# Kernel optimization log

Hardware: AMD Instinct MI355X
Metric: run time of the kernel (lower is better)

Reference implementation:

```python
import jax, jax.numpy as jnp
import numpy as np

V, P, C, M, P_ORIG, T = 81920, 131072, 512, 1024, 163840, 262144


def setup_inputs() -> dict:
    key = jax.random.key(0)
    ks = jax.random.split(key, 6)
    adapter_feat = jax.random.normal(ks[0], (V, C), dtype=jnp.float32)
    ce = jax.random.normal(ks[1], (M, C), dtype=jnp.float32)
    # caption embeddings arrive pre-normalized in the original pipeline
    caption_embed = ce / jnp.clip(jnp.linalg.norm(ce, axis=-1, keepdims=True), 1e-12)
    logit_scale = jnp.full((1,), np.log(1.0 / 0.07), dtype=jnp.float32)  # learnable param init
    v2p_map = jax.random.randint(ks[2], (P,), 0, V, dtype=jnp.int32)
    origin_idx = jax.random.randint(ks[3], (P,), 0, P_ORIG, dtype=jnp.int32)
    caption_to_point_mapping = jax.random.randint(ks[4], (T,), 0, P_ORIG, dtype=jnp.int32)
    caption_seg_idx = jnp.sort(jax.random.randint(ks[5], (T,), 0, M, dtype=jnp.int32))
    return {
        "adapter_feat": adapter_feat,
        "caption_embed": caption_embed,
        "logit_scale": logit_scale,
        "v2p_map": v2p_map,
        "origin_idx": origin_idx,
        "caption_to_point_mapping": caption_to_point_mapping,
        "caption_seg_idx": caption_seg_idx,
        "n_origin_points": P_ORIG,
    }


def reference(adapter_feat, caption_embed, logit_scale, v2p_map, origin_idx,
              caption_to_point_mapping, caption_seg_idx, n_origin_points):
    n_pts = v2p_map.shape[0]
    n_captions = caption_embed.shape[0]

    # gather voxel features to points, L2-normalize (feat_norm=True)
    feats = adapter_feat[v2p_map]                                       # [P, C]
    feats = feats / jnp.clip(jnp.linalg.norm(feats, axis=-1, keepdims=True), 1e-12)

    # per-point log-softmax caption scores
    logits = (feats @ caption_embed.T) * jnp.exp(logit_scale[0])        # [P, M]
    scores = jax.nn.log_softmax(logits, axis=-1)                        # [P, M]

    # origin-point -> current-point mapping; -1 where origin point was dropped
    ptom = jnp.full((n_origin_points,), -1, dtype=jnp.int32)
    ptom = ptom.at[origin_idx].set(jnp.arange(n_pts, dtype=jnp.int32))

    gidx = ptom[caption_to_point_mapping]                               # [T]
    invalid = (gidx < 0).astype(scores.dtype)                           # [T]
    # torch negative advanced indexing wraps; replicate faithfully
    safe = jnp.where(gidx < 0, gidx + n_pts, gidx)
    gathered = scores[safe]                                             # [T, M]

    # scatter-sum scores and counts per caption segment
    pooled = jax.ops.segment_sum(gathered, caption_seg_idx, num_segments=n_captions)
    cnt = jax.ops.segment_sum(jnp.ones_like(invalid), caption_seg_idx, num_segments=n_captions)
    ninv = jax.ops.segment_sum(invalid, caption_seg_idx, num_segments=n_captions)
    real_n_points = cnt - ninv                                          # [N]

    denom = jnp.where(real_n_points > 0,
                      1.0 / jnp.where(real_n_points > 0, real_n_points, 1.0), 0.0)
    pooled = pooled * denom[:, None]                                    # [N, M]
    if_has_pts = real_n_points > 0
    return pooled, real_n_points, if_has_pts
```

## Files before the change

kernel.cpp:

```cpp
#include <hip/hip_runtime.h>

#define P_PTS 131072
#define CDIM  512
#define MCAP  1024
#define TLEN  262144
#define PORIG 163840

typedef unsigned short u16;
typedef unsigned char  u8;
typedef __attribute__((ext_vector_type(8))) short short8;
typedef __attribute__((ext_vector_type(4))) float f32x4;
typedef __attribute__((ext_vector_type(8))) int int8v;
typedef __attribute__((ext_vector_type(4))) int int4v;

__device__ __forceinline__ u16 f2bf(float f) {
    unsigned u = __float_as_uint(f);
    unsigned r = (u + 0x7FFFu + ((u >> 16) & 1u)) >> 16;
    return (u16)r;
}
__device__ __forceinline__ float d_e4m3(unsigned x) {
    float f = __uint_as_float((x & 0x7Fu) << 20) * 0x1p120f;
    return __uint_as_float(__float_as_uint(f) | ((x & 0x80u) << 24));
}
__device__ __forceinline__ void ld16(const void* g, void* l) {
    __builtin_amdgcn_global_load_lds(
        (const __attribute__((address_space(1))) void*)g,
        (__attribute__((address_space(3))) void*)l, 16, 0, 0);
}

__global__ __launch_bounds__(256) void prep(const float* __restrict__ cap,
                                            const int* __restrict__ oidx,
                                            u16* __restrict__ capb,
                                            u8* __restrict__ cap8,
                                            int* __restrict__ ptom,
                                            float* __restrict__ lse_sum) {
    int b = blockIdx.x, tid = threadIdx.x;
    if (b < 512) {
        int i = (b * 256 + tid) * 4;
        float4 v = *(const float4*)(cap + i);
        u16* o = capb + i;
        o[0] = f2bf(v.x); o[1] = f2bf(v.y); o[2] = f2bf(v.z); o[3] = f2bf(v.w);
        int p = __builtin_amdgcn_cvt_pk_fp8_f32(v.x, v.y, 0, false);
        p = __builtin_amdgcn_cvt_pk_fp8_f32(v.z, v.w, p, true);
        *(int*)(cap8 + i) = p;
        int t = b * 256 + tid;
        atomicMax(&ptom[oidx[t]], t);
    } else {
        int j = (b - 512) * 256 + tid;
        lse_sum[j] = 0.0f;
    }
}

__global__ __launch_bounds__(256) void gather_normalize(
    const float* __restrict__ adapter, const int* __restrict__ v2p,
    u8* __restrict__ feats8) {
    int p = blockIdx.x * 4 + (threadIdx.x >> 6);
    int lane = threadIdx.x & 63;
    int vrow = v2p[p];
    const float4* src = (const float4*)(adapter + (size_t)vrow * CDIM);
    float4 x0 = src[lane * 2];
    float4 x1 = src[lane * 2 + 1];
    float ss = x0.x*x0.x + x0.y*x0.y + x0.z*x0.z + x0.w*x0.w
             + x1.x*x1.x + x1.y*x1.y + x1.z*x1.z + x1.w*x1.w;
    #pragma unroll
    for (int off = 32; off >= 1; off >>= 1) ss += __shfl_xor(ss, off, 64);
    float inv = 1.0f / fmaxf(sqrtf(ss), 1e-12f);
    int lo = __builtin_amdgcn_cvt_pk_fp8_f32(x0.x*inv, x0.y*inv, 0, false);
    lo = __builtin_amdgcn_cvt_pk_fp8_f32(x0.z*inv, x0.w*inv, lo, true);
    int hi = __builtin_amdgcn_cvt_pk_fp8_f32(x1.x*inv, x1.y*inv, 0, false);
    hi = __builtin_amdgcn_cvt_pk_fp8_f32(x1.z*inv, x1.w*inv, hi, true);
    uint2 w; w.x = (unsigned)lo; w.y = (unsigned)hi;
    *(uint2*)(feats8 + (size_t)p * CDIM + lane * 8) = w;
}

__global__ __launch_bounds__(256) void make_rows(const int* __restrict__ ctpm,
                                                 const int* __restrict__ ptom,
                                                 unsigned* __restrict__ rows) {
    int t = blockIdx.x * 256 + threadIdx.x;
    int g = ptom[ctpm[t]];
    rows[t] = (g < 0) ? ((unsigned)(g + P_PTS) | 0x80000000u) : (unsigned)g;
}

__global__ __launch_bounds__(256) void lse_gemm(
    const u8* __restrict__ feats8, const u8* __restrict__ cap8,
    const float* __restrict__ lsc, float* __restrict__ lse_sum) {
    __shared__ __align__(16) u8 As[16384];
    __shared__ __align__(16) u8 Bs[16384];
    const int tid  = threadIdx.x;
    const int wave = tid >> 6;
    const int lane = tid & 63;
    const unsigned id = blockIdx.x;
    const int col0 = (int)((id >> 3) & 7u) * 128;
    const int row0 = (int)((id & 7u) + 8u * (id >> 6)) * 128;
    const int wm = (wave >> 1) * 64;
    const int wn = (wave & 1) * 64;
    const float sf = __expf(lsc[0]);

    f32x4 acc[4][4] = {};

    const int srow = tid >> 3;
    const int kc   = (tid & 7) ^ (srow & 7);
    const u8* gA = feats8 + (size_t)(row0 + srow) * CDIM + kc * 16;
    const u8* gB = cap8   + (size_t)(col0 + srow) * CDIM + kc * 16;
    u8* lA = As + wave * 1024;
    u8* lB = Bs + wave * 1024;

    const int m = lane & 15;
    const int q = lane >> 4;
    const u8* rA1 = As + (size_t)((wm + m) * 8 + ((2*q)   ^ (m & 7))) * 16;
    const u8* rA2 = As + (size_t)((wm + m) * 8 + ((2*q+1) ^ (m & 7))) * 16;
    const u8* rB1 = Bs + (size_t)((wn + m) * 8 + ((2*q)   ^ (m & 7))) * 16;
    const u8* rB2 = Bs + (size_t)((wn + m) * 8 + ((2*q+1) ^ (m & 7))) * 16;

    #pragma unroll
    for (int k0 = 0; k0 < CDIM; k0 += 128) {
        __syncthreads();
        #pragma unroll
        for (int c = 0; c < 4; ++c) {
            ld16(gA + (size_t)c * 32 * CDIM + k0, lA + c * 4096);
            ld16(gB + (size_t)c * 32 * CDIM + k0, lB + c * 4096);
        }
        __syncthreads();
        int8v af[4], bv[4];
        #pragma unroll
        for (int i = 0; i < 4; ++i) {
            int4v lo = *(const int4v*)(rA1 + i * 2048);
            int4v hi = *(const int4v*)(rA2 + i * 2048);
            af[i][0]=lo[0]; af[i][1]=lo[1]; af[i][2]=lo[2]; af[i][3]=lo[3];
            af[i][4]=hi[0]; af[i][5]=hi[1]; af[i][6]=hi[2]; af[i][7]=hi[3];
        }
        #pragma unroll
        for (int j = 0; j < 4; ++j) {
            int4v lo = *(const int4v*)(rB1 + j * 2048);
            int4v hi = *(const int4v*)(rB2 + j * 2048);
            bv[j][0]=lo[0]; bv[j][1]=lo[1]; bv[j][2]=lo[2]; bv[j][3]=lo[3];
            bv[j][4]=hi[0]; bv[j][5]=hi[1]; bv[j][6]=hi[2]; bv[j][7]=hi[3];
        }
        #pragma unroll
        for (int i = 0; i < 4; ++i)
            #pragma unroll
            for (int j = 0; j < 4; ++j)
                acc[i][j] = __builtin_amdgcn_mfma_scale_f32_16x16x128_f8f6f4(
                    af[i], bv[j], acc[i][j], 0, 0, 0, 127, 0, 127);
    }

    #pragma unroll
    for (int i = 0; i < 4; ++i) {
        float s4[4] = {0.f, 0.f, 0.f, 0.f};
        #pragma unroll
        for (int j = 0; j < 4; ++j)
            #pragma unroll
            for (int r = 0; r < 4; ++r)
                s4[r] += __expf(acc[i][j][r] * sf - sf);
        #pragma unroll
        for (int off = 8; off >= 1; off >>= 1)
            #pragma unroll
            for (int r = 0; r < 4; ++r)
                s4[r] += __shfl_xor(s4[r], off, 64);
        if (m == 0) {
            int rbase = row0 + wm + i * 16 + q * 4;
            #pragma unroll
            for (int r = 0; r < 4; ++r)
                atomicAdd(&lse_sum[rbase + r], s4[r]);
        }
    }
}

__device__ __forceinline__ int lower_bound(const int* __restrict__ a, int n, int key) {
    int lo = 0, hi = n;
    while (lo < hi) { int mid = (lo + hi) >> 1; if (a[mid] < key) lo = mid + 1; else hi = mid; }
    return lo;
}

__global__ __launch_bounds__(1024) void seg_reduce(
    const u8* __restrict__ feats8, const float* __restrict__ lse_sum,
    const unsigned* __restrict__ rows, const int* __restrict__ seg,
    const float* __restrict__ lsc,
    u16* __restrict__ Fb, float* __restrict__ Lout, float* __restrict__ realn) {
    int s = blockIdx.x;
    int tid = threadIdx.x, wave = tid >> 6, lane = tid & 63;
    int start = lower_bound(seg, TLEN, s);
    int end   = lower_bound(seg, TLEN, s + 1);
    float a[8] = {0,0,0,0,0,0,0,0};
    float Lacc = 0.f; int inv = 0;
    int r = start + wave;
    for (; r + 16 < end; r += 32) {
        unsigned p0 = rows[r], p1 = rows[r + 16];
        int r0 = (int)(p0 & 0x7FFFFFFFu), r1 = (int)(p1 & 0x7FFFFFFFu);
        uint2 v0 = *(const uint2*)(feats8 + (size_t)r0 * CDIM + lane * 8);
        uint2 v1 = *(const uint2*)(feats8 + (size_t)r1 * CDIM + lane * 8);
        if (lane == 0) {
            inv += (int)(p0 >> 31) + (int)(p1 >> 31);
            Lacc += __logf(lse_sum[r0]) + __logf(lse_sum[r1]);
        }
        a[0] += d_e4m3(v0.x);       a[1] += d_e4m3(v0.x >> 8);
        a[2] += d_e4m3(v0.x >> 16); a[3] += d_e4m3(v0.x >> 24);
        a[4] += d_e4m3(v0.y);       a[5] += d_e4m3(v0.y >> 8);
        a[6] += d_e4m3(v0.y >> 16); a[7] += d_e4m3(v0.y >> 24);
        a[0] += d_e4m3(v1.x);       a[1] += d_e4m3(v1.x >> 8);
        a[2] += d_e4m3(v1.x >> 16); a[3] += d_e4m3(v1.x >> 24);
        a[4] += d_e4m3(v1.y);       a[5] += d_e4m3(v1.y >> 8);
        a[6] += d_e4m3(v1.y >> 16); a[7] += d_e4m3(v1.y >> 24);
    }
    if (r < end) {
        unsigned p0 = rows[r];
        int r0 = (int)(p0 & 0x7FFFFFFFu);
        uint2 v0 = *(const uint2*)(feats8 + (size_t)r0 * CDIM + lane * 8);
        if (lane == 0) { inv += (int)(p0 >> 31); Lacc += __logf(lse_sum[r0]); }
        a[0] += d_e4m3(v0.x);       a[1] += d_e4m3(v0.x >> 8);
        a[2] += d_e4m3(v0.x >> 16); a[3] += d_e4m3(v0.x >> 24);
        a[4] += d_e4m3(v0.y);       a[5] += d_e4m3(v0.y >> 8);
        a[6] += d_e4m3(v0.y >> 16); a[7] += d_e4m3(v0.y >> 24);
    }
    __shared__ float pF[16][512];
    __shared__ float pL[16];
    __shared__ int   pI[16];
    #pragma unroll
    for (int u = 0; u < 8; ++u) pF[wave][lane * 8 + u] = a[u];
    if (lane == 0) { pL[wave] = Lacc; pI[wave] = inv; }
    __syncthreads();
    if (tid < 512) {
        float f = 0.f;
        #pragma unroll
        for (int w = 0; w < 16; ++w) f += pF[w][tid];
        Fb[(size_t)s * CDIM + tid] = f2bf(f);
    }
    if (tid == 0) {
        float cnt = (float)(end - start);
        float Ls = 0.f; int ninv = 0;
        #pragma unroll
        for (int w = 0; w < 16; ++w) { Ls += pL[w]; ninv += pI[w]; }
        realn[s] = cnt - (float)ninv;
        Lout[s] = Ls + __expf(lsc[0]) * cnt;
    }
}

__global__ __launch_bounds__(256) void pooled_gemm(
    const u16* __restrict__ Fb, const u16* __restrict__ capb,
    const float* __restrict__ Lout, const float* __restrict__ realn,
    const float* __restrict__ lsc, float* __restrict__ out) {
    __shared__ __align__(16) u16 As[64 * 32];
    __shared__ __align__(16) u16 Bs[64 * 32];
    const int tid  = threadIdx.x;
    const int wave = tid >> 6;
    const int lane = tid & 63;
    const int col0 = blockIdx.x * 64;
    const int row0 = blockIdx.y * 64;
    const int wm = (wave >> 1) * 32;
    const int wn = (wave & 1) * 32;
    const float sf = __expf(lsc[0]);
    f32x4 acc[2][2] = {};
    const int srow = tid >> 2;
    const int scol = (tid & 3) * 8;
    const u16* gA0 = Fb   + (size_t)(row0 + srow) * CDIM + scol;
    const u16* gB0 = capb + (size_t)(col0 + srow) * CDIM + scol;
    u16* lA0 = As + wave * 512;
    u16* lB0 = Bs + wave * 512;
    const int mrow = lane & 15;
    const int quad = lane >> 4;
    const u16* rA = As + (wm + mrow) * 32 + quad * 8;
    const u16* rB = Bs + (wn + mrow) * 32 + quad * 8;
    #pragma unroll 4
    for (int k0 = 0; k0 < CDIM; k0 += 32) {
        __syncthreads();
        ld16(gA0 + k0, lA0);
        ld16(gB0 + k0, lB0);
        __syncthreads();
        short8 af[2], bfr[2];
        #pragma unroll
        for (int i = 0; i < 2; ++i) af[i]  = *(const short8*)(rA + i * 512);
        #pragma unroll
        for (int j = 0; j < 2; ++j) bfr[j] = *(const short8*)(rB + j * 512);
        #pragma unroll
        for (int i = 0; i < 2; ++i)
            #pragma unroll
            for (int j = 0; j < 2; ++j)
                acc[i][j] = __builtin_amdgcn_mfma_f32_16x16x32_bf16(
                    af[i], bfr[j], acc[i][j], 0, 0, 0);
    }
    #pragma unroll
    for (int i = 0; i < 2; ++i) {
        #pragma unroll
        for (int r = 0; r < 4; ++r) {
            int s = row0 + wm + i * 16 + quad * 4 + r;
            float rn = realn[s];
            float dn = rn > 0.f ? 1.0f / rn : 0.0f;
            float L = Lout[s];
            #pragma unroll
            for (int j = 0; j < 2; ++j) {
                int mc = col0 + wn + j * 16 + mrow;
                out[(size_t)s * MCAP + mc] = (sf * acc[i][j][r] - L) * dn;
            }
        }
    }
    if (col0 == 0 && tid < 64) {
        int s = row0 + tid;
        float rv = realn[s];
        out[MCAP * MCAP + s] = rv;
        out[MCAP * MCAP + MCAP + s] = (rv > 0.f) ? 1.0f : 0.0f;
    }
}

extern "C" void kernel_launch(void* const* d_in, const int* in_sizes, int n_in,
                              void* d_out, int out_size, void* d_ws, size_t ws_size,
                              hipStream_t stream) {
    const float* adapter = (const float*)d_in[0];
    const float* cap     = (const float*)d_in[1];
    const float* lsc     = (const float*)d_in[2];
    const int*   v2p     = (const int*)d_in[3];
    const int*   oidx    = (const int*)d_in[4];
    const int*   ctpm    = (const int*)d_in[5];
    const int*   seg     = (const int*)d_in[6];
    float* out = (float*)d_out;

    char* ws = (char*)d_ws;
    u8*       feats8  = (u8*)(ws);
    u8*       cap8    = (u8*)(ws + 67108864);
    u16*      capb    = (u16*)(ws + 67633152);
    float*    lse_sum = (float*)(ws + 68681728);
    int*      ptom    = (int*)(ws + 69206016);
    unsigned* rows    = (unsigned*)(ws + 69861376);
    u16*      Fb      = (u16*)(ws + 70909952);
    float*    Lout    = (float*)(ws + 71958528);
    float*    realn   = (float*)(ws + 71962624);

    hipMemsetAsync(ptom, 0xFF, (size_t)PORIG * 4, stream);

    prep<<<1024, 256, 0, stream>>>(cap, oidx, capb, cap8, ptom, lse_sum);
    gather_normalize<<<P_PTS / 4, 256, 0, stream>>>(adapter, v2p, feats8);
    make_rows<<<TLEN / 256, 256, 0, stream>>>(ctpm, ptom, rows);
    lse_gemm<<<(P_PTS / 128) * (MCAP / 128), 256, 0, stream>>>(feats8, cap8, lsc, lse_sum);
    seg_reduce<<<MCAP, 1024, 0, stream>>>(feats8, lse_sum, rows, seg, lsc, Fb, Lout, realn);
    pooled_gemm<<<dim3(MCAP / 64, MCAP / 64), 256, 0, stream>>>(Fb, capb, Lout, realn, lsc, out);
}
```

Before: 410.2 us.

## Fuse prep kernels and pre-swizzle caption fp8 into MFMA register layout

Merges the gather/normalize, caption conversion and lse_sum zeroing into one launch. The make_rows work moves into extra blocks of the lse_gemm launch. Caption embeddings are pre-converted to fp8 in the exact per-lane MFMA operand layout, so the GEMM loads B fragments directly from global memory instead of staging them through LDS. This cuts launch count and halves LDS traffic and shared memory per block, at the cost of uncoalesced-ish global B loads issued before the barrier and a larger mixed-role prep kernel.

```diff
diff --git a/kernel.cpp b/kernel.cpp
--- a/kernel.cpp
+++ b/kernel.cpp
@@ -28,72 +28,83 @@
         (__attribute__((address_space(3))) void*)l, 16, 0, 0);
 }
 
-__global__ __launch_bounds__(256) void prep(const float* __restrict__ cap,
-                                            const int* __restrict__ oidx,
-                                            u16* __restrict__ capb,
-                                            u8* __restrict__ cap8,
-                                            int* __restrict__ ptom,
-                                            float* __restrict__ lse_sum) {
+__global__ __launch_bounds__(256) void gather_prep(
+    const float* __restrict__ adapter, const int* __restrict__ v2p,
+    const float* __restrict__ cap, const int* __restrict__ oidx,
+    u8* __restrict__ feats8, u16* __restrict__ capb, u8* __restrict__ Bswz,
+    int* __restrict__ ptom, float* __restrict__ lse_sum) {
     int b = blockIdx.x, tid = threadIdx.x;
-    if (b < 512) {
-        int i = (b * 256 + tid) * 4;
+    if (b < 32768) {
+        int p = b * 4 + (tid >> 6);
+        int lane = tid & 63;
+        int vrow = v2p[p];
+        const float4* src = (const float4*)(adapter + (size_t)vrow * CDIM);
+        float4 x0 = src[lane * 2];
+        float4 x1 = src[lane * 2 + 1];
+        float ss = x0.x*x0.x + x0.y*x0.y + x0.z*x0.z + x0.w*x0.w
+                 + x1.x*x1.x + x1.y*x1.y + x1.z*x1.z + x1.w*x1.w;
+        #pragma unroll
+        for (int off = 32; off >= 1; off >>= 1) ss += __shfl_xor(ss, off, 64);
+        float inv = 1.0f / fmaxf(sqrtf(ss), 1e-12f);
+        int lo = __builtin_amdgcn_cvt_pk_fp8_f32(x0.x*inv, x0.y*inv, 0, false);
+        lo = __builtin_amdgcn_cvt_pk_fp8_f32(x0.z*inv, x0.w*inv, lo, true);
+        int hi = __builtin_amdgcn_cvt_pk_fp8_f32(x1.x*inv, x1.y*inv, 0, false);
+        hi = __builtin_amdgcn_cvt_pk_fp8_f32(x1.z*inv, x1.w*inv, hi, true);
+        uint2 w; w.x = (unsigned)lo; w.y = (unsigned)hi;
+        *(uint2*)(feats8 + (size_t)p * CDIM + lane * 8) = w;
+    } else if (b < 33280) {
+        int t = (b - 32768) * 256 + tid;
+        int i = t * 4;
         float4 v = *(const float4*)(cap + i);
         u16* o = capb + i;
         o[0] = f2bf(v.x); o[1] = f2bf(v.y); o[2] = f2bf(v.z); o[3] = f2bf(v.w);
-        int p = __builtin_amdgcn_cvt_pk_fp8_f32(v.x, v.y, 0, false);
-        p = __builtin_amdgcn_cvt_pk_fp8_f32(v.z, v.w, p, true);
-        *(int*)(cap8 + i) = p;
-        int t = b * 256 + tid;
         atomicMax(&ptom[oidx[t]], t);
+    } else if (b < 33792) {
+        int j = (b - 33280) * 256 + tid;
+        lse_sum[j] = 0.0f;
     } else {
-        int j = (b - 512) * 256 + tid;
-        lse_sum[j] = 0.0f;
-    }
-}
-
-__global__ __launch_bounds__(256) void gather_normalize(
-    const float* __restrict__ adapter, const int* __restrict__ v2p,
-    u8* __restrict__ feats8) {
-    int p = blockIdx.x * 4 + (threadIdx.x >> 6);
-    int lane = threadIdx.x & 63;
-    int vrow = v2p[p];
-    const float4* src = (const float4*)(adapter + (size_t)vrow * CDIM);
-    float4 x0 = src[lane * 2];
-    float4 x1 = src[lane * 2 + 1];
-    float ss = x0.x*x0.x + x0.y*x0.y + x0.z*x0.z + x0.w*x0.w
-             + x1.x*x1.x + x1.y*x1.y + x1.z*x1.z + x1.w*x1.w;
-    #pragma unroll
-    for (int off = 32; off >= 1; off >>= 1) ss += __shfl_xor(ss, off, 64);
-    float inv = 1.0f / fmaxf(sqrtf(ss), 1e-12f);
-    int lo = __builtin_amdgcn_cvt_pk_fp8_f32(x0.x*inv, x0.y*inv, 0, false);
-    lo = __builtin_amdgcn_cvt_pk_fp8_f32(x0.z*inv, x0.w*inv, lo, true);
-    int hi = __builtin_amdgcn_cvt_pk_fp8_f32(x1.x*inv, x1.y*inv, 0, false);
-    hi = __builtin_amdgcn_cvt_pk_fp8_f32(x1.z*inv, x1.w*inv, hi, true);
-    uint2 w; w.x = (unsigned)lo; w.y = (unsigned)hi;
-    *(uint2*)(feats8 + (size_t)p * CDIM + lane * 8) = w;
-}
-
-__global__ __launch_bounds__(256) void make_rows(const int* __restrict__ ctpm,
-                                                 const int* __restrict__ ptom,
-                                                 unsigned* __restrict__ rows) {
-    int t = blockIdx.x * 256 + threadIdx.x;
-    int g = ptom[ctpm[t]];
-    rows[t] = (g < 0) ? ((unsigned)(g + P_PTS) | 0x80000000u) : (unsigned)g;
+        int g2 = (b - 33792) * 256 + tid;
+        int c    = g2 & 1;
+        int lane = (g2 >> 1) & 63;
+        int j    = (g2 >> 7) & 3;
+        int kk   = (g2 >> 9) & 3;
+        int wn   = (g2 >> 11) & 1;
+        int c0   = g2 >> 12;
+        int col  = c0 * 128 + wn * 64 + j * 16 + (lane & 15);
+        int kb   = kk * 128 + (lane >> 4) * 32 + c * 16;
+        const float* s = cap + (size_t)col * CDIM + kb;
+        unsigned w4[4];
+        #pragma unroll
+        for (int u = 0; u < 4; ++u) {
+            int p = __builtin_amdgcn_cvt_pk_fp8_f32(s[u*4+0], s[u*4+1], 0, false);
+            p = __builtin_amdgcn_cvt_pk_fp8_f32(s[u*4+2], s[u*4+3], p, true);
+            w4[u] = (unsigned)p;
+        }
+        *(uint4*)(Bswz + (size_t)g2 * 16) = *(uint4*)w4;
+    }
 }
 
 __global__ __launch_bounds__(256) void lse_gemm(
-    const u8* __restrict__ feats8, const u8* __restrict__ cap8,
-    const float* __restrict__ lsc, float* __restrict__ lse_sum) {
+    const u8* __restrict__ feats8, const u8* __restrict__ Bswz,
+    const float* __restrict__ lsc, float* __restrict__ lse_sum,
+    const int* __restrict__ ctpm, const int* __restrict__ ptom,
+    unsigned* __restrict__ rows) {
+    if (blockIdx.x >= 8192) {
+        int t = (blockIdx.x - 8192) * 256 + threadIdx.x;
+        int g = ptom[ctpm[t]];
+        rows[t] = (g < 0) ? ((unsigned)(g + P_PTS) | 0x80000000u) : (unsigned)g;
+        return;
+    }
     __shared__ __align__(16) u8 As[16384];
-    __shared__ __align__(16) u8 Bs[16384];
     const int tid  = threadIdx.x;
     const int wave = tid >> 6;
     const int lane = tid & 63;
     const unsigned id = blockIdx.x;
-    const int col0 = (int)((id >> 3) & 7u) * 128;
+    const int c0   = (int)((id >> 3) & 7u);
+    const int col0 = c0 * 128;
     const int row0 = (int)((id & 7u) + 8u * (id >> 6)) * 128;
     const int wm = (wave >> 1) * 64;
-    const int wn = (wave & 1) * 64;
+    const int wn1 = (wave & 1);
     const float sf = __expf(lsc[0]);
 
     f32x4 acc[4][4] = {};
@@ -101,40 +112,37 @@
     const int srow = tid >> 3;
     const int kc   = (tid & 7) ^ (srow & 7);
     const u8* gA = feats8 + (size_t)(row0 + srow) * CDIM + kc * 16;
-    const u8* gB = cap8   + (size_t)(col0 + srow) * CDIM + kc * 16;
     u8* lA = As + wave * 1024;
-    u8* lB = Bs + wave * 1024;
 
     const int m = lane & 15;
     const int q = lane >> 4;
     const u8* rA1 = As + (size_t)((wm + m) * 8 + ((2*q)   ^ (m & 7))) * 16;
     const u8* rA2 = As + (size_t)((wm + m) * 8 + ((2*q+1) ^ (m & 7))) * 16;
-    const u8* rB1 = Bs + (size_t)((wn + m) * 8 + ((2*q)   ^ (m & 7))) * 16;
-    const u8* rB2 = Bs + (size_t)((wn + m) * 8 + ((2*q+1) ^ (m & 7))) * 16;
+    const u8* bw = Bswz + (size_t)(c0 * 2 + wn1) * 16 * 2048 + lane * 32;
 
     #pragma unroll
     for (int k0 = 0; k0 < CDIM; k0 += 128) {
+        const int kk = k0 >> 7;
+        int8v bv[4];
+        #pragma unroll
+        for (int j = 0; j < 4; ++j) {
+            int4v lo = *(const int4v*)(bw + (kk * 4 + j) * 2048);
+            int4v hi = *(const int4v*)(bw + (kk * 4 + j) * 2048 + 16);
+            bv[j][0]=lo[0]; bv[j][1]=lo[1]; bv[j][2]=lo[2]; bv[j][3]=lo[3];
+            bv[j][4]=hi[0]; bv[j][5]=hi[1]; bv[j][6]=hi[2]; bv[j][7]=hi[3];
+        }
         __syncthreads();
         #pragma unroll
-        for (int c = 0; c < 4; ++c) {
+        for (int c = 0; c < 4; ++c)
             ld16(gA + (size_t)c * 32 * CDIM + k0, lA + c * 4096);
-            ld16(gB + (size_t)c * 32 * CDIM + k0, lB + c * 4096);
-        }
         __syncthreads();
-        int8v af[4], bv[4];
+        int8v af[4];
         #pragma unroll
         for (int i = 0; i < 4; ++i) {
             int4v lo = *(const int4v*)(rA1 + i * 2048);
             int4v hi = *(const int4v*)(rA2 + i * 2048);
             af[i][0]=lo[0]; af[i][1]=lo[1]; af[i][2]=lo[2]; af[i][3]=lo[3];
             af[i][4]=hi[0]; af[i][5]=hi[1]; af[i][6]=hi[2]; af[i][7]=hi[3];
-        }
-        #pragma unroll
-        for (int j = 0; j < 4; ++j) {
-            int4v lo = *(const int4v*)(rB1 + j * 2048);
-            int4v hi = *(const int4v*)(rB2 + j * 2048);
-            bv[j][0]=lo[0]; bv[j][1]=lo[1]; bv[j][2]=lo[2]; bv[j][3]=lo[3];
-            bv[j][4]=hi[0]; bv[j][5]=hi[1]; bv[j][6]=hi[2]; bv[j][7]=hi[3];
         }
         #pragma unroll
         for (int i = 0; i < 4; ++i)
@@ -315,8 +323,8 @@
 
     char* ws = (char*)d_ws;
     u8*       feats8  = (u8*)(ws);
-    u8*       cap8    = (u8*)(ws + 67108864);
-    u16*      capb    = (u16*)(ws + 67633152);
+    u16*      capb    = (u16*)(ws + 67108864);
+    u8*       Bswz    = (u8*)(ws + 68157440);
     float*    lse_sum = (float*)(ws + 68681728);
     int*      ptom    = (int*)(ws + 69206016);
     unsigned* rows    = (unsigned*)(ws + 69861376);
@@ -326,10 +334,10 @@
 
     hipMemsetAsync(ptom, 0xFF, (size_t)PORIG * 4, stream);
 
-    prep<<<1024, 256, 0, stream>>>(cap, oidx, capb, cap8, ptom, lse_sum);
-    gather_normalize<<<P_PTS / 4, 256, 0, stream>>>(adapter, v2p, feats8);
-    make_rows<<<TLEN / 256, 256, 0, stream>>>(ctpm, ptom, rows);
-    lse_gemm<<<(P_PTS / 128) * (MCAP / 128), 256, 0, stream>>>(feats8, cap8, lsc, lse_sum);
+    gather_prep<<<33920, 256, 0, stream>>>(adapter, v2p, cap, oidx,
+                                           feats8, capb, Bswz, ptom, lse_sum);
+    lse_gemm<<<8192 + TLEN / 256, 256, 0, stream>>>(feats8, Bswz, lsc, lse_sum,
+                                                    ctpm, ptom, rows);
     seg_reduce<<<MCAP, 1024, 0, stream>>>(feats8, lse_sum, rows, seg, lsc, Fb, Lout, realn);
     pooled_gemm<<<dim3(MCAP / 64, MCAP / 64), 256, 0, stream>>>(Fb, capb, Lout, realn, lsc, out);
 }
```

Result: no change. 403.8 us (-1.6%).
